# Performance work log

Hardware: AMD Instinct MI355X
Metric: run time of the kernel (lower is better)

Reference implementation:

```python
import jax, jax.numpy as jnp
import numpy as np

B, L, C, H = 32, 512, 512, 8
DH = C // H
LN_EPS = 1e-5


def setup_inputs() -> dict:
    key = jax.random.key(0)
    ks = jax.random.split(key, 5)
    x = jax.random.normal(ks[0], (B, L, C), dtype=jnp.float32)
    # nn.Linear weights are (out, in); y = x @ W.T
    wq = jax.random.normal(ks[1], (C, C), dtype=jnp.float32) * 0.02
    wk = jax.random.normal(ks[2], (C, C), dtype=jnp.float32) * 0.02
    wv = jax.random.normal(ks[3], (C, C), dtype=jnp.float32) * 0.02
    # source zero-inits the bias table; use small randoms so it actually contributes
    bias_table = jax.random.normal(ks[4], (2 * L - 1, H), dtype=jnp.float32) * 0.02
    gamma = jnp.ones((C,), dtype=jnp.float32)
    beta = jnp.zeros((C,), dtype=jnp.float32)
    coords = np.arange(L)
    rel_index = jnp.asarray(coords[None, :] - coords[:, None] + (L - 1), dtype=jnp.int32)  # (L, L)
    return {"x": x, "wq": wq, "wk": wk, "wv": wv, "bias_table": bias_table,
            "gamma": gamma, "beta": beta, "rel_index": rel_index}


def reference(x, wq, wk, wv, bias_table, gamma, beta, rel_index):
    Bx, Lx, Cx = x.shape
    scale = Cx ** (-0.5)  # note: scale uses full emb_size, as in source
    q = (x @ wq.T).reshape(Bx, Lx, H, DH).transpose(0, 2, 1, 3)  # (B,H,L,Dh)
    k = (x @ wk.T).reshape(Bx, Lx, H, DH).transpose(0, 2, 1, 3)
    v = (x @ wv.T).reshape(Bx, Lx, H, DH).transpose(0, 2, 1, 3)
    attn = jax.nn.softmax(jnp.einsum('bhqd,bhkd->bhqk', q, k) * scale, axis=-1)
    # post-softmax relative bias gather-add
    rel_bias = bias_table[rel_index]                # (L, L, H)
    attn = attn + rel_bias.transpose(2, 0, 1)[None]  # (1,H,L,L) broadcast
    out = jnp.einsum('bhqk,bhkd->bhqd', attn, v)
    out = out.transpose(0, 2, 1, 3).reshape(Bx, Lx, Cx)
    mu = out.mean(axis=-1, keepdims=True)
    var = jnp.mean(jnp.square(out - mu), axis=-1, keepdims=True)
    return gamma * (out - mu) * jax.lax.rsqrt(var + LN_EPS) + beta
```

## Files before the change

### kernel.cpp

```cpp
#include <hip/hip_runtime.h>
#include <hip/hip_bf16.h>

typedef unsigned short u16;
typedef __attribute__((ext_vector_type(8))) __bf16 bf16x8;
typedef __attribute__((ext_vector_type(4))) float f32x4;

#define BB 32
#define LL 512
#define CC 512
#define HH 8
#define DH 64
#define MROWS (BB * LL)
#define NQKV  (3 * CC)

#define XB_BYTES ((size_t)MROWS * CC * 2)
#define WC_BYTES ((size_t)NQKV * CC * 2)
#define QKV_OFF  (XB_BYTES + WC_BYTES)

#define SCALE2 (0.044194173824159216f * 1.4426950408889634f)

__device__ inline u16 f2b(float f) {
  union { float f; unsigned u; } a; a.f = f;
  unsigned u = a.u;
  return (u16)((u + 0x7FFFu + ((u >> 16) & 1u)) >> 16);
}

__device__ inline unsigned pack2(float a, float b) {
  float2 f; f.x = a; f.y = b;
  union { __hip_bfloat162 h; unsigned u; } c;
  c.h = __float22bfloat162_rn(f);
  return c.u;
}

__global__ __launch_bounds__(256) void cvt_x(const float* __restrict__ x, u16* __restrict__ xb) {
  int i = blockIdx.x * 256 + threadIdx.x;
  float4 v = ((const float4*)x)[i];
  uint2 o; o.x = pack2(v.x, v.y); o.y = pack2(v.z, v.w);
  ((uint2*)xb)[i] = o;
}

__global__ __launch_bounds__(256) void cvt_w(const float* __restrict__ wq, const float* __restrict__ wk,
                                             const float* __restrict__ wv, u16* __restrict__ wcat) {
  int i = blockIdx.x * 256 + threadIdx.x;
  int e = i * 4;
  int n = e >> 9;
  int k = e & 511;
  const float* src = (n < 512) ? (wq + (size_t)n * 512)
                   : (n < 1024) ? (wk + (size_t)(n - 512) * 512)
                                : (wv + (size_t)(n - 1024) * 512);
  const float sc = (n < 512) ? SCALE2 : 1.0f;
  float4 v = *(const float4*)(src + k);
  uint2 o; o.x = pack2(v.x * sc, v.y * sc); o.y = pack2(v.z * sc, v.w * sc);
  *(uint2*)(wcat + (size_t)n * 512 + k) = o;
}

typedef __attribute__((address_space(1))) void* as1_void_p;
typedef __attribute__((address_space(3))) void* as3_void_p;

__device__ inline void async16(const u16* g, u16* l) {
#if __has_builtin(__builtin_amdgcn_global_load_lds)
  __builtin_amdgcn_global_load_lds((as1_void_p)g, (as3_void_p)l, 16, 0, 0);
#else
  *(uint4*)l = *(const uint4*)g;
#endif
}

__global__ __launch_bounds__(256) void gemm_qkv(const u16* __restrict__ A, const u16* __restrict__ Bw,
                                                u16* __restrict__ Cm) {
  __shared__ u16 a_lds[128 * 32];
  __shared__ u16 b_lds[128 * 32];
  const int n0 = blockIdx.x * 128, m0 = blockIdx.y * 128;
  const int t = threadIdx.x, l = t & 63;
  const int wrow = ((t >> 7) & 1) * 64, wcol = ((t >> 6) & 1) * 64;
  const int lr = l & 15, lq = l >> 4;

  f32x4 acc[4][4] = {};

  for (int k0 = 0; k0 < 512; k0 += 32) {
    {
      int c0 = t, c1 = t + 256;
      async16(A  + (size_t)(m0 + (c0 >> 2)) * 512 + k0 + (c0 & 3) * 8, &a_lds[c0 * 8]);
      async16(A  + (size_t)(m0 + (c1 >> 2)) * 512 + k0 + (c1 & 3) * 8, &a_lds[c1 * 8]);
      async16(Bw + (size_t)(n0 + (c0 >> 2)) * 512 + k0 + (c0 & 3) * 8, &b_lds[c0 * 8]);
      async16(Bw + (size_t)(n0 + (c1 >> 2)) * 512 + k0 + (c1 & 3) * 8, &b_lds[c1 * 8]);
    }
    __syncthreads();
    bf16x8 af[4], bfr[4];
#pragma unroll
    for (int r = 0; r < 4; ++r) af[r]  = *(const bf16x8*)&a_lds[(wrow + r * 16 + lr) * 32 + lq * 8];
#pragma unroll
    for (int c = 0; c < 4; ++c) bfr[c] = *(const bf16x8*)&b_lds[(wcol + c * 16 + lr) * 32 + lq * 8];
#pragma unroll
    for (int r = 0; r < 4; ++r)
#pragma unroll
      for (int c = 0; c < 4; ++c)
        acc[r][c] = __builtin_amdgcn_mfma_f32_16x16x32_bf16(af[r], bfr[c], acc[r][c], 0, 0, 0);
    __syncthreads();
  }
#pragma unroll
  for (int r = 0; r < 4; ++r) {
#pragma unroll
    for (int i = 0; i < 4; ++i) {
      int m = m0 + wrow + r * 16 + lq * 4 + i;
      u16* crow = Cm + (size_t)m * NQKV + n0 + wcol;
#pragma unroll
      for (int c = 0; c < 4; ++c)
        crow[c * 16 + lr] = f2b(acc[r][c][i]);
    }
  }
}

__global__ __launch_bounds__(256) void transpose_v(const u16* __restrict__ qkv, u16* __restrict__ vT) {
  const int bh = blockIdx.x;
  const int b = bh >> 3, h = bh & 7;
  const int lc0 = blockIdx.y * 128;
  __shared__ u16 tile[32 * 72];
  const int t = threadIdx.x;
  for (int lc = lc0; lc < lc0 + 128; lc += 32) {
    int lrow = t >> 3, dcol = (t & 7) * 8;
    const u16* src = qkv + (size_t)(b * 512 + lc + lrow) * NQKV + 1024 + h * 64 + dcol;
    *(uint4*)&tile[lrow * 72 + dcol] = *(const uint4*)src;
    __syncthreads();
    int d = t >> 2, lp = (t & 3) * 8;
    union { ushort4 v4[2]; u16 s[8]; } tmp;
#pragma unroll
    for (int j = 0; j < 8; ++j) tmp.s[j] = tile[(lp + j) * 72 + d];
    *(uint4*)&vT[(size_t)(bh * 64 + d) * 512 + lc + lp] = *(uint4*)&tmp;
    __syncthreads();
  }
}

__global__ __launch_bounds__(256) void attn_kernel(const u16* __restrict__ qkv, const u16* __restrict__ vT,
                                                   const float* __restrict__ bias_table,
                                                   float* __restrict__ out) {
  __shared__ u16 p_lds[32 * 512];
  __shared__ float bias_lds[544];
  __shared__ float reds[4][32];

  const int flat = blockIdx.x;
  const int bh = ((flat >> 7) << 3) | (flat & 7);
  const int q0 = ((flat >> 3) & 15) * 32;
  const int b = bh >> 3, h = bh & 7;
  const int t = threadIdx.x, l = t & 63, w = t >> 6;
  const int lr = l & 15, lq = l >> 4;

  {
    const int rel0 = 480 - q0;
    for (int i = t; i < 543; i += 256)
      bias_lds[i] = bias_table[(size_t)(rel0 + i) * HH + h];
  }

  bf16x8 bq[2][2];
#pragma unroll
  for (int qt = 0; qt < 2; ++qt) {
    const u16* qrow = qkv + (size_t)(b * 512 + q0 + qt * 16 + lr) * NQKV + h * 64;
    bq[qt][0] = *(const bf16x8*)(qrow + lq * 8);
    bq[qt][1] = *(const bf16x8*)(qrow + 32 + lq * 8);
  }

  f32x4 sT[2][8];
#pragma unroll
  for (int ct = 0; ct < 8; ++ct) {
    const int kcol = w * 128 + ct * 16;
    const u16* krow = qkv + (size_t)(b * 512 + kcol + lr) * NQKV + 512 + h * 64;
    bf16x8 ak0 = *(const bf16x8*)(krow + lq * 8);
    bf16x8 ak1 = *(const bf16x8*)(krow + 32 + lq * 8);
#pragma unroll
    for (int qt = 0; qt < 2; ++qt) {
      f32x4 acc = {0.f, 0.f, 0.f, 0.f};
      acc = __builtin_amdgcn_mfma_f32_16x16x32_bf16(ak0, bq[qt][0], acc, 0, 0, 0);
      acc = __builtin_amdgcn_mfma_f32_16x16x32_bf16(ak1, bq[qt][1], acc, 0, 0, 0);
      sT[qt][ct] = acc;
    }
  }

  float sloc[2];
#pragma unroll
  for (int qt = 0; qt < 2; ++qt) {
    float s = 0.f;
#pragma unroll
    for (int ct = 0; ct < 8; ++ct)
#pragma unroll
      for (int i = 0; i < 4; ++i) {
        float e = exp2f(sT[qt][ct][i]);
        sT[qt][ct][i] = e;
        s += e;
      }
    s += __shfl_xor(s, 16, 64);
    s += __shfl_xor(s, 32, 64);
    sloc[qt] = s;
  }
  if (lq == 0) { reds[w][lr] = sloc[0]; reds[w][16 + lr] = sloc[1]; }
  __syncthreads();
  float rinv[2];
#pragma unroll
  for (int qt = 0; qt < 2; ++qt)
    rinv[qt] = 1.0f / (reds[0][qt * 16 + lr] + reds[1][qt * 16 + lr] +
                       reds[2][qt * 16 + lr] + reds[3][qt * 16 + lr]);

#pragma unroll
  for (int qt = 0; qt < 2; ++qt) {
    const int qlocal = qt * 16 + lr;
    u16* prow = p_lds + qlocal * 512;
    const int boff = w * 128 + lq * 4 + 31 - qlocal;
#pragma unroll
    for (int ct = 0; ct < 8; ++ct) {
      const int gsw = w * 8 + (ct ^ (lr & 7));
      float p0 = sT[qt][ct][0] * rinv[qt] + bias_lds[boff + ct * 16 + 0];
      float p1 = sT[qt][ct][1] * rinv[qt] + bias_lds[boff + ct * 16 + 1];
      float p2 = sT[qt][ct][2] * rinv[qt] + bias_lds[boff + ct * 16 + 2];
      float p3 = sT[qt][ct][3] * rinv[qt] + bias_lds[boff + ct * 16 + 3];
      uint2 pk; pk.x = pack2(p0, p1); pk.y = pack2(p2, p3);
      *(uint2*)&prow[gsw * 16 + lq * 4] = pk;
    }
  }
  __syncthreads();

  f32x4 accP[2] = {};
  const u16* vrow = vT + (size_t)(bh * 64 + w * 16 + lr) * 512;
#pragma unroll
  for (int kb = 0; kb < 16; ++kb) {
    bf16x8 av = *(const bf16x8*)(vrow + kb * 32 + lq * 8);
    const int g = 2 * kb + (lq >> 1);
    const int off = ((g & ~7) | ((g & 7) ^ (lr & 7))) * 16 + (lq & 1) * 8;
#pragma unroll
    for (int qt = 0; qt < 2; ++qt) {
      bf16x8 bp = *(const bf16x8*)&p_lds[(qt * 16 + lr) * 512 + off];
      accP[qt] = __builtin_amdgcn_mfma_f32_16x16x32_bf16(av, bp, accP[qt], 0, 0, 0);
    }
  }
#pragma unroll
  for (int qt = 0; qt < 2; ++qt)
    *(f32x4*)&out[(size_t)(b * 512 + q0 + qt * 16 + lr) * 512 + h * 64 + w * 16 + lq * 4] = accP[qt];
}

__global__ __launch_bounds__(256) void ln_kernel(float* __restrict__ out,
                                                 const float* __restrict__ gamma,
                                                 const float* __restrict__ beta) {
  const int t = threadIdx.x;
  const int r2 = t >> 7;
  const int row = blockIdx.x * 2 + r2;
  const int c = (t & 127) * 4;
  float* p = out + (size_t)row * 512;
  float4 v = *(float4*)(p + c);
  float s = v.x + v.y + v.z + v.w;
  float s2 = v.x * v.x + v.y * v.y + v.z * v.z + v.w * v.w;
#pragma unroll
  for (int d = 1; d < 64; d <<= 1) { s += __shfl_xor(s, d, 64); s2 += __shfl_xor(s2, d, 64); }
  __shared__ float ps[4], ps2[4];
  const int wv = t >> 6;
  if ((t & 63) == 0) { ps[wv] = s; ps2[wv] = s2; }
  __syncthreads();
  s  = ps[r2 * 2]  + ps[r2 * 2 + 1];
  s2 = ps2[r2 * 2] + ps2[r2 * 2 + 1];
  float mu = s * (1.0f / 512.0f);
  float var = s2 * (1.0f / 512.0f) - mu * mu;
  float rs = rsqrtf(var + 1e-5f);
  float4 g = *(const float4*)(gamma + c);
  float4 bb = *(const float4*)(beta + c);
  v.x = g.x * (v.x - mu) * rs + bb.x;
  v.y = g.y * (v.y - mu) * rs + bb.y;
  v.z = g.z * (v.z - mu) * rs + bb.z;
  v.w = g.w * (v.w - mu) * rs + bb.w;
  *(float4*)(p + c) = v;
}

extern "C" void kernel_launch(void* const* d_in, const int* in_sizes, int n_in,
                              void* d_out, int out_size, void* d_ws, size_t ws_size,
                              hipStream_t stream) {
  const float* x    = (const float*)d_in[0];
  const float* wq   = (const float*)d_in[1];
  const float* wk   = (const float*)d_in[2];
  const float* wv   = (const float*)d_in[3];
  const float* bias = (const float*)d_in[4];
  const float* gamma = (const float*)d_in[5];
  const float* beta  = (const float*)d_in[6];
  float* out = (float*)d_out;

  char* ws = (char*)d_ws;
  u16* xb   = (u16*)ws;
  u16* wcat = (u16*)(ws + XB_BYTES);
  u16* qkv  = (u16*)(ws + QKV_OFF);
  u16* vT   = xb;

  cvt_x<<<dim3((MROWS * CC) / 4 / 256), 256, 0, stream>>>(x, xb);
  cvt_w<<<dim3((NQKV * CC) / 4 / 256), 256, 0, stream>>>(wq, wk, wv, wcat);
  gemm_qkv<<<dim3(NQKV / 128, MROWS / 128), 256, 0, stream>>>(xb, wcat, qkv);
  transpose_v<<<dim3(256, 4), 256, 0, stream>>>(qkv, vT);
  attn_kernel<<<dim3(16 * 256), 256, 0, stream>>>(qkv, vT, bias, out);
  ln_kernel<<<dim3(MROWS / 2), 256, 0, stream>>>(out, gamma, beta);
}
```

Measured before the change: 232.3 us.

## Fuse attention with layernorm by looping all heads per 16-row query tile

Replaces the per-head attention kernel and the separate layernorm kernel with one kernel. Each block takes 16 query rows of one batch, loops over all 8 heads, keeps the output rows in registers and applies layernorm before a single write. This removes the fp32 write-then-read round trip of the attention output and one launch. In exchange the query tile shrinks from 32 to 16 rows, so K and V are re-read twice as often per query. The grid is four times smaller and runs the heads serially, with several barriers per head.

```diff
diff --git a/kernel.cpp b/kernel.cpp
--- a/kernel.cpp
+++ b/kernel.cpp
@@ -130,139 +130,111 @@
   }
 }
 
-__global__ __launch_bounds__(256) void attn_kernel(const u16* __restrict__ qkv, const u16* __restrict__ vT,
-                                                   const float* __restrict__ bias_table,
-                                                   float* __restrict__ out) {
-  __shared__ u16 p_lds[32 * 512];
-  __shared__ float bias_lds[544];
-  __shared__ float reds[4][32];
+__global__ __launch_bounds__(256) void attn_ln(const u16* __restrict__ qkv, const u16* __restrict__ vT,
+                                               const float* __restrict__ bias_table,
+                                               const float* __restrict__ gamma,
+                                               const float* __restrict__ beta,
+                                               float* __restrict__ out) {
+  __shared__ u16 p_lds[16 * 512];
+  __shared__ float bias_lds[528];
+  __shared__ float redA[4][16], redB[4][16];
 
   const int flat = blockIdx.x;
-  const int bh = ((flat >> 7) << 3) | (flat & 7);
-  const int q0 = ((flat >> 3) & 15) * 32;
-  const int b = bh >> 3, h = bh & 7;
+  const int b = (flat & 7) | ((flat >> 8) << 3);
+  const int q0 = ((flat >> 3) & 31) * 16;
   const int t = threadIdx.x, l = t & 63, w = t >> 6;
   const int lr = l & 15, lq = l >> 4;
-
-  {
-    const int rel0 = 480 - q0;
-    for (int i = t; i < 543; i += 256)
+  const int rel0 = 496 - q0;
+
+  f32x4 ocol[8] = {};
+
+  for (int h = 0; h < 8; ++h) {
+    for (int i = t; i < 527; i += 256)
       bias_lds[i] = bias_table[(size_t)(rel0 + i) * HH + h];
-  }
-
-  bf16x8 bq[2][2];
-#pragma unroll
-  for (int qt = 0; qt < 2; ++qt) {
-    const u16* qrow = qkv + (size_t)(b * 512 + q0 + qt * 16 + lr) * NQKV + h * 64;
-    bq[qt][0] = *(const bf16x8*)(qrow + lq * 8);
-    bq[qt][1] = *(const bf16x8*)(qrow + 32 + lq * 8);
-  }
-
-  f32x4 sT[2][8];
-#pragma unroll
-  for (int ct = 0; ct < 8; ++ct) {
-    const int kcol = w * 128 + ct * 16;
-    const u16* krow = qkv + (size_t)(b * 512 + kcol + lr) * NQKV + 512 + h * 64;
-    bf16x8 ak0 = *(const bf16x8*)(krow + lq * 8);
-    bf16x8 ak1 = *(const bf16x8*)(krow + 32 + lq * 8);
-#pragma unroll
-    for (int qt = 0; qt < 2; ++qt) {
+
+    const u16* qrow = qkv + (size_t)(b * 512 + q0 + lr) * NQKV + h * 64;
+    bf16x8 bq0 = *(const bf16x8*)(qrow + lq * 8);
+    bf16x8 bq1 = *(const bf16x8*)(qrow + 32 + lq * 8);
+
+    f32x4 sT[8];
+#pragma unroll
+    for (int ct = 0; ct < 8; ++ct) {
+      const int kcol = w * 128 + ct * 16;
+      const u16* krow = qkv + (size_t)(b * 512 + kcol + lr) * NQKV + 512 + h * 64;
+      bf16x8 ak0 = *(const bf16x8*)(krow + lq * 8);
+      bf16x8 ak1 = *(const bf16x8*)(krow + 32 + lq * 8);
       f32x4 acc = {0.f, 0.f, 0.f, 0.f};
-      acc = __builtin_amdgcn_mfma_f32_16x16x32_bf16(ak0, bq[qt][0], acc, 0, 0, 0);
-      acc = __builtin_amdgcn_mfma_f32_16x16x32_bf16(ak1, bq[qt][1], acc, 0, 0, 0);
-      sT[qt][ct] = acc;
-    }
-  }
-
-  float sloc[2];
-#pragma unroll
-  for (int qt = 0; qt < 2; ++qt) {
+      acc = __builtin_amdgcn_mfma_f32_16x16x32_bf16(ak0, bq0, acc, 0, 0, 0);
+      acc = __builtin_amdgcn_mfma_f32_16x16x32_bf16(ak1, bq1, acc, 0, 0, 0);
+      sT[ct] = acc;
+    }
+
     float s = 0.f;
 #pragma unroll
     for (int ct = 0; ct < 8; ++ct)
 #pragma unroll
       for (int i = 0; i < 4; ++i) {
-        float e = exp2f(sT[qt][ct][i]);
-        sT[qt][ct][i] = e;
+        float e = exp2f(sT[ct][i]);
+        sT[ct][i] = e;
         s += e;
       }
     s += __shfl_xor(s, 16, 64);
     s += __shfl_xor(s, 32, 64);
-    sloc[qt] = s;
-  }
-  if (lq == 0) { reds[w][lr] = sloc[0]; reds[w][16 + lr] = sloc[1]; }
-  __syncthreads();
-  float rinv[2];
-#pragma unroll
-  for (int qt = 0; qt < 2; ++qt)
-    rinv[qt] = 1.0f / (reds[0][qt * 16 + lr] + reds[1][qt * 16 + lr] +
-                       reds[2][qt * 16 + lr] + reds[3][qt * 16 + lr]);
-
-#pragma unroll
-  for (int qt = 0; qt < 2; ++qt) {
-    const int qlocal = qt * 16 + lr;
-    u16* prow = p_lds + qlocal * 512;
-    const int boff = w * 128 + lq * 4 + 31 - qlocal;
+    if (lq == 0) redA[w][lr] = s;
+    __syncthreads();
+    const float rinv = 1.0f / (redA[0][lr] + redA[1][lr] + redA[2][lr] + redA[3][lr]);
+
+    u16* prow = p_lds + lr * 512;
+    const int boff = w * 128 + lq * 4 + 15 - lr;
 #pragma unroll
     for (int ct = 0; ct < 8; ++ct) {
       const int gsw = w * 8 + (ct ^ (lr & 7));
-      float p0 = sT[qt][ct][0] * rinv[qt] + bias_lds[boff + ct * 16 + 0];
-      float p1 = sT[qt][ct][1] * rinv[qt] + bias_lds[boff + ct * 16 + 1];
-      float p2 = sT[qt][ct][2] * rinv[qt] + bias_lds[boff + ct * 16 + 2];
-      float p3 = sT[qt][ct][3] * rinv[qt] + bias_lds[boff + ct * 16 + 3];
+      float p0 = sT[ct][0] * rinv + bias_lds[boff + ct * 16 + 0];
+      float p1 = sT[ct][1] * rinv + bias_lds[boff + ct * 16 + 1];
+      float p2 = sT[ct][2] * rinv + bias_lds[boff + ct * 16 + 2];
+      float p3 = sT[ct][3] * rinv + bias_lds[boff + ct * 16 + 3];
       uint2 pk; pk.x = pack2(p0, p1); pk.y = pack2(p2, p3);
       *(uint2*)&prow[gsw * 16 + lq * 4] = pk;
     }
-  }
+    __syncthreads();
+
+    const u16* vrow = vT + (size_t)((b * 8 + h) * 64 + w * 16 + lr) * 512;
+#pragma unroll
+    for (int kb = 0; kb < 16; ++kb) {
+      bf16x8 av = *(const bf16x8*)(vrow + kb * 32 + lq * 8);
+      const int g = 2 * kb + (lq >> 1);
+      const int off = ((g & ~7) | ((g & 7) ^ (lr & 7))) * 16 + (lq & 1) * 8;
+      bf16x8 bp = *(const bf16x8*)&p_lds[lr * 512 + off];
+      ocol[h] = __builtin_amdgcn_mfma_f32_16x16x32_bf16(av, bp, ocol[h], 0, 0, 0);
+    }
+  }
+
+  float s = 0.f, s2 = 0.f;
+#pragma unroll
+  for (int h = 0; h < 8; ++h)
+#pragma unroll
+    for (int i = 0; i < 4; ++i) { float v = ocol[h][i]; s += v; s2 += v * v; }
+  s  += __shfl_xor(s, 16, 64);  s  += __shfl_xor(s, 32, 64);
+  s2 += __shfl_xor(s2, 16, 64); s2 += __shfl_xor(s2, 32, 64);
+  if (lq == 0) { redA[w][lr] = s; redB[w][lr] = s2; }
   __syncthreads();
-
-  f32x4 accP[2] = {};
-  const u16* vrow = vT + (size_t)(bh * 64 + w * 16 + lr) * 512;
-#pragma unroll
-  for (int kb = 0; kb < 16; ++kb) {
-    bf16x8 av = *(const bf16x8*)(vrow + kb * 32 + lq * 8);
-    const int g = 2 * kb + (lq >> 1);
-    const int off = ((g & ~7) | ((g & 7) ^ (lr & 7))) * 16 + (lq & 1) * 8;
-#pragma unroll
-    for (int qt = 0; qt < 2; ++qt) {
-      bf16x8 bp = *(const bf16x8*)&p_lds[(qt * 16 + lr) * 512 + off];
-      accP[qt] = __builtin_amdgcn_mfma_f32_16x16x32_bf16(av, bp, accP[qt], 0, 0, 0);
-    }
-  }
-#pragma unroll
-  for (int qt = 0; qt < 2; ++qt)
-    *(f32x4*)&out[(size_t)(b * 512 + q0 + qt * 16 + lr) * 512 + h * 64 + w * 16 + lq * 4] = accP[qt];
-}
-
-__global__ __launch_bounds__(256) void ln_kernel(float* __restrict__ out,
-                                                 const float* __restrict__ gamma,
-                                                 const float* __restrict__ beta) {
-  const int t = threadIdx.x;
-  const int r2 = t >> 7;
-  const int row = blockIdx.x * 2 + r2;
-  const int c = (t & 127) * 4;
-  float* p = out + (size_t)row * 512;
-  float4 v = *(float4*)(p + c);
-  float s = v.x + v.y + v.z + v.w;
-  float s2 = v.x * v.x + v.y * v.y + v.z * v.z + v.w * v.w;
-#pragma unroll
-  for (int d = 1; d < 64; d <<= 1) { s += __shfl_xor(s, d, 64); s2 += __shfl_xor(s2, d, 64); }
-  __shared__ float ps[4], ps2[4];
-  const int wv = t >> 6;
-  if ((t & 63) == 0) { ps[wv] = s; ps2[wv] = s2; }
-  __syncthreads();
-  s  = ps[r2 * 2]  + ps[r2 * 2 + 1];
-  s2 = ps2[r2 * 2] + ps2[r2 * 2 + 1];
-  float mu = s * (1.0f / 512.0f);
-  float var = s2 * (1.0f / 512.0f) - mu * mu;
-  float rs = rsqrtf(var + 1e-5f);
-  float4 g = *(const float4*)(gamma + c);
-  float4 bb = *(const float4*)(beta + c);
-  v.x = g.x * (v.x - mu) * rs + bb.x;
-  v.y = g.y * (v.y - mu) * rs + bb.y;
-  v.z = g.z * (v.z - mu) * rs + bb.z;
-  v.w = g.w * (v.w - mu) * rs + bb.w;
-  *(float4*)(p + c) = v;
+  s  = redA[0][lr] + redA[1][lr] + redA[2][lr] + redA[3][lr];
+  s2 = redB[0][lr] + redB[1][lr] + redB[2][lr] + redB[3][lr];
+  const float mu = s * (1.0f / 512.0f);
+  const float var = s2 * (1.0f / 512.0f) - mu * mu;
+  const float rs = rsqrtf(var + 1e-5f);
+
+  float* orow = out + (size_t)(b * 512 + q0 + lr) * 512;
+#pragma unroll
+  for (int h = 0; h < 8; ++h) {
+    const int c = h * 64 + w * 16 + lq * 4;
+    f32x4 g = *(const f32x4*)(gamma + c);
+    f32x4 be = *(const f32x4*)(beta + c);
+    f32x4 o;
+#pragma unroll
+    for (int i = 0; i < 4; ++i) o[i] = g[i] * (ocol[h][i] - mu) * rs + be[i];
+    *(f32x4*)(orow + c) = o;
+  }
 }
 
 extern "C" void kernel_launch(void* const* d_in, const int* in_sizes, int n_in,
@@ -287,6 +259,5 @@
   cvt_w<<<dim3((NQKV * CC) / 4 / 256), 256, 0, stream>>>(wq, wk, wv, wcat);
   gemm_qkv<<<dim3(NQKV / 128, MROWS / 128), 256, 0, stream>>>(xb, wcat, qkv);
   transpose_v<<<dim3(256, 4), 256, 0, stream>>>(qkv, vT);
-  attn_kernel<<<dim3(16 * 256), 256, 0, stream>>>(qkv, vT, bias, out);
-  ln_kernel<<<dim3(MROWS / 2), 256, 0, stream>>>(out, gamma, beta);
-}
+  attn_ln<<<dim3(BB * (LL / 16)), 256, 0, stream>>>(qkv, vT, bias, gamma, beta, out);
+}
```

Measured after the change: 311.9 us. +34.3%, slower.

## Stream attention per wave over key blocks and apply bias via separate MFMA

Applied to the files above, without the earlier changes.

Restructures the attention kernel so each wave owns 16 query rows and streams through all 512 keys. It computes exp scores, packs them through a small per-wave LDS tile and accumulates P·V on the fly, with normalization deferred to the end. The relative bias is no longer added to P in LDS. Instead a second accumulator multiplies bias values, read as truncated bf16 high halves straight from the fp32 table, by V, and the result is added after scaling. This removes the 32 KB P buffer and the block-wide barriers to raise occupancy, at the cost of doubling the PV MFMAs, having every wave re-read the full K and V for its head, and using strided global gathers for the bias.

```diff
diff --git a/kernel.cpp b/kernel.cpp
--- a/kernel.cpp
+++ b/kernel.cpp
@@ -133,105 +133,77 @@
 __global__ __launch_bounds__(256) void attn_kernel(const u16* __restrict__ qkv, const u16* __restrict__ vT,
                                                    const float* __restrict__ bias_table,
                                                    float* __restrict__ out) {
-  __shared__ u16 p_lds[32 * 512];
-  __shared__ float bias_lds[544];
-  __shared__ float reds[4][32];
-
+  __shared__ u16 p_lds[4][16 * 40];
   const int flat = blockIdx.x;
-  const int bh = ((flat >> 7) << 3) | (flat & 7);
-  const int q0 = ((flat >> 3) & 15) * 32;
-  const int b = bh >> 3, h = bh & 7;
-  const int t = threadIdx.x, l = t & 63, w = t >> 6;
+  const int h = flat & 7, qg = (flat >> 3) & 7, b = flat >> 6;
+  const int t = threadIdx.x, w = t >> 6, l = t & 63;
   const int lr = l & 15, lq = l >> 4;
-
-  {
-    const int rel0 = 480 - q0;
-    for (int i = t; i < 543; i += 256)
-      bias_lds[i] = bias_table[(size_t)(rel0 + i) * HH + h];
-  }
-
-  bf16x8 bq[2][2];
-#pragma unroll
-  for (int qt = 0; qt < 2; ++qt) {
-    const u16* qrow = qkv + (size_t)(b * 512 + q0 + qt * 16 + lr) * NQKV + h * 64;
-    bq[qt][0] = *(const bf16x8*)(qrow + lq * 8);
-    bq[qt][1] = *(const bf16x8*)(qrow + 32 + lq * 8);
-  }
-
-  f32x4 sT[2][8];
-#pragma unroll
-  for (int ct = 0; ct < 8; ++ct) {
-    const int kcol = w * 128 + ct * 16;
-    const u16* krow = qkv + (size_t)(b * 512 + kcol + lr) * NQKV + 512 + h * 64;
-    bf16x8 ak0 = *(const bf16x8*)(krow + lq * 8);
-    bf16x8 ak1 = *(const bf16x8*)(krow + 32 + lq * 8);
-#pragma unroll
-    for (int qt = 0; qt < 2; ++qt) {
-      f32x4 acc = {0.f, 0.f, 0.f, 0.f};
-      acc = __builtin_amdgcn_mfma_f32_16x16x32_bf16(ak0, bq[qt][0], acc, 0, 0, 0);
-      acc = __builtin_amdgcn_mfma_f32_16x16x32_bf16(ak1, bq[qt][1], acc, 0, 0, 0);
-      sT[qt][ct] = acc;
+  const int q0 = (qg * 4 + w) * 16;
+
+  const u16* qrow = qkv + (size_t)(b * 512 + q0 + lr) * NQKV + h * 64;
+  bf16x8 bq0 = *(const bf16x8*)(qrow + lq * 8);
+  bf16x8 bq1 = *(const bf16x8*)(qrow + 32 + lq * 8);
+
+  u16* ps = p_lds[w];
+  const u16* tb = (const u16*)bias_table + (size_t)(511 - q0 - lr) * 16 + h * 2 + 1;
+  const u16* kbase = qkv + (size_t)(b * 512) * NQKV + 512 + h * 64;
+  const u16* vbase = vT + (size_t)((b * 8 + h) * 64) * 512;
+
+  f32x4 accP[4] = {}, accB[4] = {};
+  float ssum = 0.f;
+
+#pragma unroll 2
+  for (int kb = 0; kb < 16; ++kb) {
+    const u16* k0 = kbase + (size_t)(kb * 32 + lr) * NQKV;
+    const u16* k1 = k0 + (size_t)16 * NQKV;
+    bf16x8 a00 = *(const bf16x8*)(k0 + lq * 8);
+    bf16x8 a01 = *(const bf16x8*)(k0 + 32 + lq * 8);
+    bf16x8 a10 = *(const bf16x8*)(k1 + lq * 8);
+    bf16x8 a11 = *(const bf16x8*)(k1 + 32 + lq * 8);
+    f32x4 s0 = {0.f, 0.f, 0.f, 0.f}, s1 = {0.f, 0.f, 0.f, 0.f};
+    s0 = __builtin_amdgcn_mfma_f32_16x16x32_bf16(a00, bq0, s0, 0, 0, 0);
+    s0 = __builtin_amdgcn_mfma_f32_16x16x32_bf16(a01, bq1, s0, 0, 0, 0);
+    s1 = __builtin_amdgcn_mfma_f32_16x16x32_bf16(a10, bq0, s1, 0, 0, 0);
+    s1 = __builtin_amdgcn_mfma_f32_16x16x32_bf16(a11, bq1, s1, 0, 0, 0);
+
+    float e0[4], e1[4];
+#pragma unroll
+    for (int i = 0; i < 4; ++i) { e0[i] = exp2f(s0[i]); e1[i] = exp2f(s1[i]); }
+#pragma unroll
+    for (int i = 0; i < 4; ++i) ssum += e0[i] + e1[i];
+
+    uint2 pk0, pk1;
+    pk0.x = pack2(e0[0], e0[1]); pk0.y = pack2(e0[2], e0[3]);
+    pk1.x = pack2(e1[0], e1[1]); pk1.y = pack2(e1[2], e1[3]);
+    *(uint2*)&ps[lr * 40 + lq * 4] = pk0;
+    *(uint2*)&ps[lr * 40 + 16 + lq * 4] = pk1;
+    bf16x8 bp = *(const bf16x8*)&ps[lr * 40 + lq * 8];
+
+    union { bf16x8 v; u16 s[8]; } bfr;
+    const u16* tkb = tb + (size_t)(kb * 32 + lq * 8) * 16;
+#pragma unroll
+    for (int j = 0; j < 8; ++j) bfr.s[j] = tkb[j * 16];
+
+#pragma unroll
+    for (int dt = 0; dt < 4; ++dt) {
+      bf16x8 av = *(const bf16x8*)(vbase + (size_t)(dt * 16 + lr) * 512 + kb * 32 + lq * 8);
+      accP[dt] = __builtin_amdgcn_mfma_f32_16x16x32_bf16(av, bp, accP[dt], 0, 0, 0);
+      accB[dt] = __builtin_amdgcn_mfma_f32_16x16x32_bf16(av, bfr.v, accB[dt], 0, 0, 0);
     }
   }
 
-  float sloc[2];
-#pragma unroll
-  for (int qt = 0; qt < 2; ++qt) {
-    float s = 0.f;
-#pragma unroll
-    for (int ct = 0; ct < 8; ++ct)
-#pragma unroll
-      for (int i = 0; i < 4; ++i) {
-        float e = exp2f(sT[qt][ct][i]);
-        sT[qt][ct][i] = e;
-        s += e;
-      }
-    s += __shfl_xor(s, 16, 64);
-    s += __shfl_xor(s, 32, 64);
-    sloc[qt] = s;
-  }
-  if (lq == 0) { reds[w][lr] = sloc[0]; reds[w][16 + lr] = sloc[1]; }
-  __syncthreads();
-  float rinv[2];
-#pragma unroll
-  for (int qt = 0; qt < 2; ++qt)
-    rinv[qt] = 1.0f / (reds[0][qt * 16 + lr] + reds[1][qt * 16 + lr] +
-                       reds[2][qt * 16 + lr] + reds[3][qt * 16 + lr]);
-
-#pragma unroll
-  for (int qt = 0; qt < 2; ++qt) {
-    const int qlocal = qt * 16 + lr;
-    u16* prow = p_lds + qlocal * 512;
-    const int boff = w * 128 + lq * 4 + 31 - qlocal;
-#pragma unroll
-    for (int ct = 0; ct < 8; ++ct) {
-      const int gsw = w * 8 + (ct ^ (lr & 7));
-      float p0 = sT[qt][ct][0] * rinv[qt] + bias_lds[boff + ct * 16 + 0];
-      float p1 = sT[qt][ct][1] * rinv[qt] + bias_lds[boff + ct * 16 + 1];
-      float p2 = sT[qt][ct][2] * rinv[qt] + bias_lds[boff + ct * 16 + 2];
-      float p3 = sT[qt][ct][3] * rinv[qt] + bias_lds[boff + ct * 16 + 3];
-      uint2 pk; pk.x = pack2(p0, p1); pk.y = pack2(p2, p3);
-      *(uint2*)&prow[gsw * 16 + lq * 4] = pk;
-    }
-  }
-  __syncthreads();
-
-  f32x4 accP[2] = {};
-  const u16* vrow = vT + (size_t)(bh * 64 + w * 16 + lr) * 512;
-#pragma unroll
-  for (int kb = 0; kb < 16; ++kb) {
-    bf16x8 av = *(const bf16x8*)(vrow + kb * 32 + lq * 8);
-    const int g = 2 * kb + (lq >> 1);
-    const int off = ((g & ~7) | ((g & 7) ^ (lr & 7))) * 16 + (lq & 1) * 8;
-#pragma unroll
-    for (int qt = 0; qt < 2; ++qt) {
-      bf16x8 bp = *(const bf16x8*)&p_lds[(qt * 16 + lr) * 512 + off];
-      accP[qt] = __builtin_amdgcn_mfma_f32_16x16x32_bf16(av, bp, accP[qt], 0, 0, 0);
-    }
-  }
-#pragma unroll
-  for (int qt = 0; qt < 2; ++qt)
-    *(f32x4*)&out[(size_t)(b * 512 + q0 + qt * 16 + lr) * 512 + h * 64 + w * 16 + lq * 4] = accP[qt];
+  ssum += __shfl_xor(ssum, 16, 64);
+  ssum += __shfl_xor(ssum, 32, 64);
+  const float rinv = 1.0f / ssum;
+
+  float* orow = out + (size_t)(b * 512 + q0 + lr) * 512 + h * 64;
+#pragma unroll
+  for (int dt = 0; dt < 4; ++dt) {
+    f32x4 o;
+#pragma unroll
+    for (int i = 0; i < 4; ++i) o[i] = accP[dt][i] * rinv + accB[dt][i];
+    *(f32x4*)(orow + dt * 16 + lq * 4) = o;
+  }
 }
 
 __global__ __launch_bounds__(256) void ln_kernel(float* __restrict__ out,
@@ -287,6 +259,6 @@
   cvt_w<<<dim3((NQKV * CC) / 4 / 256), 256, 0, stream>>>(wq, wk, wv, wcat);
   gemm_qkv<<<dim3(NQKV / 128, MROWS / 128), 256, 0, stream>>>(xb, wcat, qkv);
   transpose_v<<<dim3(256, 4), 256, 0, stream>>>(qkv, vT);
-  attn_kernel<<<dim3(16 * 256), 256, 0, stream>>>(qkv, vT, bias, out);
+  attn_kernel<<<dim3(BB * 64), 256, 0, stream>>>(qkv, vT, bias, out);
   ln_kernel<<<dim3(MROWS / 2), 256, 0, stream>>>(out, gamma, beta);
 }
```

Result: slower. 382.6 us (+64.7%).
